# Kernel optimization log

Hardware: AMD Instinct MI355X
Metric: run time of the kernel (lower is better)

The kernel has to match this reference:

```python
import math
import jax, jax.numpy as jnp
import numpy as np

D_MODEL = 768
N_HEAD = 12
N_BR = 4
DH = D_MODEL // N_HEAD          # 64
H_TOT = N_BR * N_HEAD           # 48
SCALE = math.pi / math.sqrt(3.0)
ATTNSCALE = DH ** -0.5


def _chebyshev(T, max_deg, dtype):
    # T_all[t, d] = Cheb poly T_d(x_t), x in [-1, 1]
    if T > 1:
        x = 2.0 * jnp.arange(T, dtype=dtype) / (T - 1) - 1.0
    else:
        x = jnp.zeros(1, dtype=dtype)
    cols = [jnp.ones_like(x), x]
    for _ in range(2, max_deg + 1):
        cols.append(2.0 * x * cols[-1] - cols[-2])
    return jnp.stack(cols, axis=1)  # (T, max_deg+1)


def setup_inputs() -> dict:
    key = jax.random.key(0)
    ks = jax.random.split(key, 12)
    s = 0.02
    return {
        "X": jax.random.normal(ks[0], (2, 1024, D_MODEL), jnp.float32),
        "Wq": jax.random.normal(ks[1], (D_MODEL * N_BR, D_MODEL), jnp.float32) * s,
        "bq": jax.random.normal(ks[2], (D_MODEL * N_BR,), jnp.float32) * s,
        "Wk": jax.random.normal(ks[3], (D_MODEL, D_MODEL), jnp.float32) * s,
        "bk": jax.random.normal(ks[4], (D_MODEL,), jnp.float32) * s,
        "Wv": jax.random.normal(ks[5], (D_MODEL, D_MODEL), jnp.float32) * s,
        "bv": jax.random.normal(ks[6], (D_MODEL,), jnp.float32) * s,
        "A": jax.random.normal(ks[7], (DH, DH), jnp.float32) * s,
        "id_bias": jax.random.normal(ks[8], (H_TOT, DH), jnp.float32) * s,
        "sink_scalars": jax.random.normal(ks[9], (H_TOT, 1, 1), jnp.float32) * s,
        "v_nulls": jax.random.normal(ks[10], (N_BR, D_MODEL), jnp.float32) * s,
        "Wo": jax.random.normal(ks[11], (N_BR, D_MODEL, D_MODEL), jnp.float32) * s,
        "bo": jnp.zeros((N_BR, D_MODEL), jnp.float32),
    }


def _attention(X, Wq, bq, Wk, bk, Wv, bv, A, id_bias, sink_scalars, v_nulls, Wo, bo):
    B, T, C = X.shape
    dtype = X.dtype

    # projections (torch Linear: x @ W.T + b)
    q = (X @ Wq.T + bq).reshape(B, T, H_TOT, DH).transpose(0, 2, 1, 3)   # (B,H_tot,T,Dh)
    v = (X @ Wv.T + bv).reshape(B, T, N_HEAD, DH).transpose(0, 2, 1, 3)
    v = jnp.tile(v, (1, N_BR, 1, 1))                                     # (B,H_tot,T,Dh)
    k = (X @ Wk.T + bk).reshape(B, T, N_HEAD, DH).transpose(0, 2, 1, 3)
    k = jnp.tile(k, (1, N_BR, 1, 1))

    # BiasedWedge on q
    S = (A - A.T)[None] + jax.vmap(jnp.diag)(id_bias)                    # (H_tot,Dh,Dh)
    q = q + jnp.einsum('bhtd,hde->bhte', q, S)

    # Chebyshev phase-vector rotation (custom RoPE)
    H = DH // 2
    max_deg = max(3, 2 * H)
    T_all = _chebyshev(T, max_deg, dtype)                                # (T, max_deg+1)
    frac = jnp.arange(H, dtype=dtype) / (H - 1) if H > 1 else jnp.zeros(1, dtype)
    n_f = jnp.clip(1 + jnp.round(frac * (max_deg - 2)).astype(jnp.int32), 1, max_deg - 1)
    raw1 = T_all[:, n_f]                                                 # (T,H)
    raw2 = T_all[:, n_f + 1]
    nrm = jnp.sqrt(raw1 * raw1 + raw2 * raw2 + 1e-8)
    base1 = (raw1 / nrm)[None, None]                                     # (1,1,T,H)
    base2 = (raw2 / nrm)[None, None]

    def apply_rot(x_in):
        x1, x2 = x_in[..., :H], x_in[..., H:]
        return jnp.concatenate([x1 * base1 - x2 * base2,
                                x1 * base2 + x2 * base1], axis=-1)

    q = apply_rot(q)
    k = apply_rot(k)

    # softplus-gated causal attention with learned sink
    scores = jnp.einsum('bhtd,bhsd->bhts', q, k) * ATTNSCALE             # (B,H_tot,T,T)
    key_self = jnp.maximum((k * k).sum(-1), 1e-6)                        # (B,H_tot,T)
    denom = jnp.sqrt(key_self)[:, :, None, :]
    w = jax.nn.softplus(scores / denom)
    causal = jnp.tril(jnp.ones((T, T), bool))                            # keep lower-tri
    w = jnp.where(causal, w, 0.0)
    w = w * jax.nn.sigmoid(SCALE * w)

    sinks = sink_scalars.reshape(1, H_TOT, 1, 1)                         # broadcast sink col
    alpha = 1.0 / (w.sum(-1, keepdims=True) + sinks + 1e-6)              # (B,H_tot,T,1)
    probs_tokens = w * alpha
    probs_sink = jnp.broadcast_to(sinks, (B, H_TOT, T, 1)) * alpha

    out_tokens = jnp.einsum('bhts,bhsd->bhtd', probs_tokens, v)
    v_null = v_nulls.reshape(H_TOT, DH)[None, :, None, :]                # (1,H_tot,1,Dh)
    context = out_tokens + probs_sink * v_null                           # (B,H_tot,T,Dh)

    context = context.reshape(B, N_BR, N_HEAD, T, DH)
    context = context.transpose(0, 1, 3, 2, 4).reshape(B, N_BR, T, C)
    y = jnp.einsum('bntc,ncd->bntd', context, Wo) + bo[None, :, None, :]
    return y.mean(axis=1)                                                # (B,T,C)


def reference(X, Wq, bq, Wk, bk, Wv, bv, A, id_bias, sink_scalars, v_nulls, Wo, bo):
    return _attention(X, Wq, bq, Wk, bk, Wv, bv, A, id_bias, sink_scalars, v_nulls, Wo, bo)
```

## Files before the change

### kernel.cpp

```cpp
#include <hip/hip_runtime.h>
#include <math.h>

#define B_ 2
#define T_ 1024
#define C_ 768
#define NH 12
#define NBR 4
#define DH_ 64
#define HT 48
#define MROWS (B_*T_)

#define SCALE_W 1.8137993642342178f
#define ATTNSCALE_ 0.125f

#define OFF_B1    0
#define OFF_B2    (OFF_B1 + 32768)
#define OFF_QKVB  (OFF_B2 + 32768)
#define OFF_BSUM  (OFF_QKVB + 4608)
#define OFF_WQKV  (OFF_BSUM + 768)
#define OFF_XB    (OFF_WQKV + 1769472)
#define OFF_WOT   (OFF_XB + 786432)
#define OFF_QF    (OFF_WOT + 1179648)
#define OFF_KF    (OFF_QF + 6291456)
#define OFF_VF    (OFF_KF + 1572864)
#define OFF_QB    OFF_KF
#define OFF_KB    (OFF_VF + 1572864)
#define OFF_VB    (OFF_KB + 786432)
#define OFF_RKS   (OFF_VB + 786432)
#define OFF_CTXB  OFF_QF

typedef __attribute__((ext_vector_type(8))) short short8t;
typedef __attribute__((ext_vector_type(4))) float f32x4;

__device__ inline ushort f2bf(float f) {
    union { float f; unsigned u; } v; v.f = f;
    unsigned r = (v.u + 0x7FFFu + ((v.u >> 16) & 1u)) >> 16;
    return (ushort)r;
}

__global__ void cheb_kernel(float* __restrict__ ws) {
    int t = blockIdx.x * 256 + threadIdx.x;
    if (t >= T_) return;
    float* b1 = ws + OFF_B1 + t * 32;
    float* b2 = ws + OFF_B2 + t * 32;
    float x = 2.0f * (float)t / 1023.0f - 1.0f;
    float Tp = 1.0f, Tc = x;
    for (int j = 0; j < 32; j++) {
        float r1 = Tc;
        float r2 = 2.0f * x * Tc - Tp;
        float nr = sqrtf(r1 * r1 + r2 * r2 + 1e-8f);
        b1[j] = r1 / nr;
        b2[j] = r2 / nr;
        Tp = r2;
        Tc = 2.0f * x * r2 - r1;
    }
}

__global__ __launch_bounds__(256) void prep_wq(
    const float* __restrict__ Aw, const float* __restrict__ idb,
    const float* __restrict__ Wq, const float* __restrict__ bq,
    float* __restrict__ ws) {
    __shared__ float Ms[64][64];
    int h = blockIdx.x;
    int tid = threadIdx.x;
    for (int i = tid; i < 4096; i += 256) {
        int d = i >> 6, e = i & 63;
        float v = Aw[d * 64 + e] - Aw[e * 64 + d];
        if (d == e) v += 1.0f + idb[h * 64 + d];
        Ms[d][e] = v;
    }
    __syncthreads();
    int c = blockIdx.y * 256 + tid;
    float wq[64];
#pragma unroll
    for (int d = 0; d < 64; d++) wq[d] = Wq[(size_t)(h * 64 + d) * 768 + c];
    ushort* EWqb = (ushort*)(ws + OFF_WQKV);
    for (int e = 0; e < 64; e++) {
        float acc = 0.f;
#pragma unroll
        for (int d = 0; d < 64; d++) acc += Ms[d][e] * wq[d];
        EWqb[(size_t)(h * 64 + e) * 768 + c] = f2bf(acc);
    }
    if (blockIdx.y == 0 && tid < 64) {
        int e = tid;
        float acc = 0.f;
        for (int d = 0; d < 64; d++) acc += Ms[d][e] * bq[h * 64 + d];
        ws[OFF_QKVB + h * 64 + e] = acc;
    }
}

__global__ void conv_bf16(const float* __restrict__ src, ushort* __restrict__ dst) {
    int i = (blockIdx.x * 256 + threadIdx.x) * 4;
    float4 v = *(const float4*)(src + i);
    ushort4 o;
    o.x = f2bf(v.x); o.y = f2bf(v.y); o.z = f2bf(v.z); o.w = f2bf(v.w);
    *(ushort4*)(dst + i) = o;
}

__global__ __launch_bounds__(256) void woT_kernel(const float* __restrict__ Wo,
                                                  ushort* __restrict__ WoT) {
    __shared__ float tile[64][65];
    int nb = blockIdx.z;
    int k0 = blockIdx.x * 64, c0 = blockIdx.y * 64;
    int tx = threadIdx.x & 63, ty = threadIdx.x >> 6;
#pragma unroll
    for (int p = 0; p < 16; p++) {
        int ky = p * 4 + ty;
        tile[ky][tx] = Wo[((size_t)nb * 768 + k0 + ky) * 768 + c0 + tx];
    }
    __syncthreads();
#pragma unroll
    for (int p = 0; p < 16; p++) {
        int cy = p * 4 + ty;
        WoT[(size_t)(c0 + cy) * 3072 + nb * 768 + k0 + tx] = f2bf(tile[tx][cy]);
    }
}

__global__ void bias_prep(const float* __restrict__ bo, const float* __restrict__ bk,
                          const float* __restrict__ bv, float* __restrict__ ws) {
    int n = blockIdx.x * 256 + threadIdx.x;
    if (n < 768) {
        ws[OFF_BSUM + n] = 0.25f * (bo[n] + bo[768 + n] + bo[1536 + n] + bo[2304 + n]);
        ws[OFF_QKVB + 3072 + n] = bk[n];
        ws[OFF_QKVB + 3840 + n] = bv[n];
    }
}

__global__ __launch_bounds__(256) void gemm_qkv(
    const ushort* __restrict__ A, const ushort* __restrict__ Bw,
    const float* __restrict__ qkvbias,
    float* __restrict__ Q, float* __restrict__ Kf, float* __restrict__ Vf) {
    __shared__ __align__(16) ushort As[128][72];
    __shared__ __align__(16) ushort Bs[128][72];
    const int K = 768;
    int tid = threadIdx.x;
    int lane = tid & 63, wid = tid >> 6;
    int wr = wid >> 1, wc = wid & 1;
    int g = lane >> 4, c = lane & 15;
    int m0 = blockIdx.x * 128, n0 = blockIdx.y * 128;
    int srow = tid >> 3;
    int scol = (tid & 7) * 8;
    f32x4 acc[4][4] = {};
    for (int k0 = 0; k0 < K; k0 += 64) {
        __syncthreads();
#pragma unroll
        for (int p = 0; p < 4; p++) {
            int r = p * 32 + srow;
            *(int4*)&As[r][scol] = *(const int4*)(A + (size_t)(m0 + r) * K + k0 + scol);
            *(int4*)&Bs[r][scol] = *(const int4*)(Bw + (size_t)(n0 + r) * K + k0 + scol);
        }
        __syncthreads();
#pragma unroll
        for (int kk = 0; kk < 2; kk++) {
            short8t af[4], bf[4];
#pragma unroll
            for (int i = 0; i < 4; i++) {
                af[i] = *(const short8t*)&As[wr * 64 + i * 16 + c][kk * 32 + g * 8];
                bf[i] = *(const short8t*)&Bs[wc * 64 + i * 16 + c][kk * 32 + g * 8];
            }
#pragma unroll
            for (int i = 0; i < 4; i++)
#pragma unroll
                for (int j = 0; j < 4; j++)
                    acc[i][j] = __builtin_amdgcn_mfma_f32_16x16x32_bf16(
                        af[i], bf[j], acc[i][j], 0, 0, 0);
        }
    }
    int y = blockIdx.y;
    float* outp; int nstr, nbase;
    if (y < 24)      { outp = Q;  nstr = 3072; nbase = 0; }
    else if (y < 30) { outp = Kf; nstr = 768;  nbase = 3072; }
    else             { outp = Vf; nstr = 768;  nbase = 3840; }
#pragma unroll
    for (int j = 0; j < 4; j++) {
        int n = n0 + wc * 64 + j * 16 + c;
        float bv = qkvbias[n];
#pragma unroll
        for (int i = 0; i < 4; i++) {
#pragma unroll
            for (int r = 0; r < 4; r++) {
                int m = m0 + wr * 64 + i * 16 + g * 4 + r;
                outp[(size_t)m * nstr + (n - nbase)] = acc[i][j][r] + bv;
            }
        }
    }
}

__global__ __launch_bounds__(256) void gemm_fin(
    const ushort* __restrict__ A, const ushort* __restrict__ Bw,
    const float* __restrict__ bsum, float* __restrict__ Y) {
    __shared__ __align__(16) ushort As[64][72];
    __shared__ __align__(16) ushort Bs[64][72];
    const int K = 3072;
    int tid = threadIdx.x;
    int lane = tid & 63, wid = tid >> 6;
    int wr = wid >> 1, wc = wid & 1;
    int g = lane >> 4, c = lane & 15;
    int m0 = blockIdx.x * 64, n0 = blockIdx.y * 64;
    int srow = tid >> 2;
    int scol = (tid & 3) * 16;
    f32x4 acc[2][2] = {};
    for (int k0 = 0; k0 < K; k0 += 64) {
        __syncthreads();
        *(int4*)&As[srow][scol]     = *(const int4*)(A + (size_t)(m0 + srow) * K + k0 + scol);
        *(int4*)&As[srow][scol + 8] = *(const int4*)(A + (size_t)(m0 + srow) * K + k0 + scol + 8);
        *(int4*)&Bs[srow][scol]     = *(const int4*)(Bw + (size_t)(n0 + srow) * K + k0 + scol);
        *(int4*)&Bs[srow][scol + 8] = *(const int4*)(Bw + (size_t)(n0 + srow) * K + k0 + scol + 8);
        __syncthreads();
#pragma unroll
        for (int kk = 0; kk < 2; kk++) {
            short8t af[2], bf[2];
#pragma unroll
            for (int i = 0; i < 2; i++) {
                af[i] = *(const short8t*)&As[wr * 32 + i * 16 + c][kk * 32 + g * 8];
                bf[i] = *(const short8t*)&Bs[wc * 32 + i * 16 + c][kk * 32 + g * 8];
            }
#pragma unroll
            for (int i = 0; i < 2; i++)
#pragma unroll
                for (int j = 0; j < 2; j++)
                    acc[i][j] = __builtin_amdgcn_mfma_f32_16x16x32_bf16(
                        af[i], bf[j], acc[i][j], 0, 0, 0);
        }
    }
#pragma unroll
    for (int j = 0; j < 2; j++) {
        int n = n0 + wc * 32 + j * 16 + c;
        float bv = bsum[n];
#pragma unroll
        for (int i = 0; i < 2; i++) {
#pragma unroll
            for (int r = 0; r < 4; r++) {
                int m = m0 + wr * 32 + i * 16 + g * 4 + r;
                Y[(size_t)m * 768 + n] = 0.25f * acc[i][j][r] + bv;
            }
        }
    }
}

__global__ void rot2_kernel(const float* __restrict__ in, int heads,
                            ushort* __restrict__ outb, float* __restrict__ rkso,
                            const float* __restrict__ ws) {
    int idx = blockIdx.x * 256 + threadIdx.x;
    if (idx >= MROWS * heads) return;
    int r = idx / heads;
    int hd = idx - r * heads;
    int tloc = r & (T_ - 1);
    int b = r >> 10;
    const float* p = in + (size_t)r * (heads * 64) + hd * 64;
    const float* b1 = ws + OFF_B1 + tloc * 32;
    const float* b2 = ws + OFF_B2 + tloc * 32;
    __align__(16) ushort ob[64];
    float nrm = 0.f;
#pragma unroll
    for (int i = 0; i < 8; i++) {
        float4 lo = *(const float4*)(p + i * 4);
        float4 hi = *(const float4*)(p + 32 + i * 4);
        float4 c1 = *(const float4*)(b1 + i * 4);
        float4 c2 = *(const float4*)(b2 + i * 4);
        float o1[4], o2[4];
        o1[0] = lo.x * c1.x - hi.x * c2.x;  o2[0] = lo.x * c2.x + hi.x * c1.x;
        o1[1] = lo.y * c1.y - hi.y * c2.y;  o2[1] = lo.y * c2.y + hi.y * c1.y;
        o1[2] = lo.z * c1.z - hi.z * c2.z;  o2[2] = lo.z * c2.z + hi.z * c1.z;
        o1[3] = lo.w * c1.w - hi.w * c2.w;  o2[3] = lo.w * c2.w + hi.w * c1.w;
#pragma unroll
        for (int j = 0; j < 4; j++) {
            ob[i * 4 + j]      = f2bf(o1[j]);
            ob[32 + i * 4 + j] = f2bf(o2[j]);
            nrm += o1[j] * o1[j] + o2[j] * o2[j];
        }
    }
    ushort* op = outb + ((size_t)(b * heads + hd) * T_ + tloc) * 64;
#pragma unroll
    for (int i = 0; i < 8; i++) *(int4*)(op + i * 8) = *(const int4*)&ob[i * 8];
    if (rkso) rkso[((b * heads + hd) << 10) + tloc] = ATTNSCALE_ / sqrtf(fmaxf(nrm, 1e-6f));
}

__global__ void vconv_kernel(const float* __restrict__ V, ushort* __restrict__ Vb) {
    int idx = blockIdx.x * 256 + threadIdx.x;
    int base = idx * 4;
    int row = base / 768, col = base - row * 768;
    int b = row >> 10, t = row & (T_ - 1);
    int hk = col >> 6, d = col & 63;
    float4 v = *(const float4*)(V + (size_t)row * 768 + col);
    ushort4 o;
    o.x = f2bf(v.x); o.y = f2bf(v.y); o.z = f2bf(v.z); o.w = f2bf(v.w);
    *(ushort4*)(Vb + ((size_t)((b * NH + hk) * T_ + t)) * 64 + d) = o;
}

__global__ __launch_bounds__(512) void attn_mfma2(
    const ushort* __restrict__ Qb, const ushort* __restrict__ Kb,
    const ushort* __restrict__ Vb, const float* __restrict__ rks,
    const float* __restrict__ sinks, const float* __restrict__ vnull,
    ushort* __restrict__ ctxb) {
    __shared__ __align__(16) ushort Ks[64][72];
    __shared__ __align__(16) ushort Vt[64][72];
    __shared__ __align__(16) ushort Ps[8][16][72];
    __shared__ float rk_s[64];
    int tid  = threadIdx.x;
    int lane = tid & 63;
    int wid  = tid >> 6;
    int p = 7 - blockIdx.x;
    int bh = blockIdx.y;
    int b = bh / HT, h = bh - b * HT;
    int hk = h % NH;
    int qt0 = p * 128;
    int g = lane >> 4;
    int c = lane & 15;
    int rowbase = qt0 + wid * 16;

    const ushort* qrow = Qb + ((size_t)(b * HT + h) * T_ + rowbase + c) * 64;
    short8t qa0 = *(const short8t*)(qrow + g * 8);
    short8t qa1 = *(const short8t*)(qrow + 32 + g * 8);

    f32x4 oacc[4] = {};
    float sumw[4] = {0.f, 0.f, 0.f, 0.f};

    const size_t kvbase = (size_t)(b * NH + hk) * T_;
    int nt = 2 * p + 2;
    int sr = tid >> 3;
    int sc = (tid & 7) * 8;
    for (int st = 0; st < nt; st++) {
        int s0 = st * 64;
        __syncthreads();
        {
            *(int4*)&Ks[sr][sc] = *(const int4*)(Kb + (kvbase + s0 + sr) * 64 + sc);
            __align__(16) ushort vv[8];
            *(int4*)&vv[0] = *(const int4*)(Vb + (kvbase + s0 + sr) * 64 + sc);
#pragma unroll
            for (int j = 0; j < 8; j++) Vt[sc + j][sr] = vv[j];
            if (tid < 64) rk_s[tid] = rks[kvbase + (size_t)s0 + tid];
        }
        __syncthreads();

        if (s0 > rowbase + 15) continue;

        f32x4 sfr[4];
#pragma unroll
        for (int f = 0; f < 4; f++) {
            f32x4 cacc = {0.f, 0.f, 0.f, 0.f};
            short8t kb0 = *(const short8t*)&Ks[f * 16 + c][g * 8];
            cacc = __builtin_amdgcn_mfma_f32_16x16x32_bf16(qa0, kb0, cacc, 0, 0, 0);
            short8t kb1 = *(const short8t*)&Ks[f * 16 + c][32 + g * 8];
            cacc = __builtin_amdgcn_mfma_f32_16x16x32_bf16(qa1, kb1, cacc, 0, 0, 0);
            sfr[f] = cacc;
        }

        bool diag = (s0 + 63 > rowbase);
#pragma unroll
        for (int f = 0; f < 4; f++) {
            int scol = f * 16 + c;
            float rkv = rk_s[scol];
#pragma unroll
            for (int r = 0; r < 4; r++) {
                int trow = g * 4 + r;
                float x = sfr[f][r] * rkv;
                float w = __logf(1.f + __expf(x));
                w = w * __builtin_amdgcn_rcpf(1.f + __expf(-SCALE_W * w));
                if (diag && s0 + scol > rowbase + trow) w = 0.f;
                sumw[r] += w;
                Ps[wid][trow][scol] = f2bf(w);
            }
        }

#pragma unroll
        for (int hf = 0; hf < 2; hf++) {
            short8t pa = *(const short8t*)&Ps[wid][c][hf * 32 + g * 8];
#pragma unroll
            for (int f = 0; f < 4; f++) {
                short8t vb = *(const short8t*)&Vt[f * 16 + c][hf * 32 + g * 8];
                oacc[f] = __builtin_amdgcn_mfma_f32_16x16x32_bf16(pa, vb, oacc[f], 0, 0, 0);
            }
        }
    }

#pragma unroll
    for (int m = 1; m < 16; m <<= 1) {
#pragma unroll
        for (int r = 0; r < 4; r++) sumw[r] += __shfl_xor(sumw[r], m, 64);
    }
    float skv = sinks[h];
    float alpha[4], ps[4];
#pragma unroll
    for (int r = 0; r < 4; r++) {
        alpha[r] = 1.0f / (sumw[r] + skv + 1e-6f);
        ps[r] = skv * alpha[r];
    }
    int nb = h / NH;
#pragma unroll
    for (int f = 0; f < 4; f++) {
        float vn = vnull[h * 64 + f * 16 + c];
#pragma unroll
        for (int r = 0; r < 4; r++) {
            int t = rowbase + g * 4 + r;
            ctxb[(size_t)(b * T_ + t) * 3072 + nb * 768 + hk * 64 + f * 16 + c]
                = f2bf(oacc[f][r] * alpha[r] + ps[r] * vn);
        }
    }
}

extern "C" void kernel_launch(void* const* d_in, const int* in_sizes, int n_in,
                              void* d_out, int out_size, void* d_ws, size_t ws_size,
                              hipStream_t stream) {
    const float* X   = (const float*)d_in[0];
    const float* Wq  = (const float*)d_in[1];
    const float* bq  = (const float*)d_in[2];
    const float* Wk  = (const float*)d_in[3];
    const float* bk  = (const float*)d_in[4];
    const float* Wv  = (const float*)d_in[5];
    const float* bv  = (const float*)d_in[6];
    const float* Aw  = (const float*)d_in[7];
    const float* idb = (const float*)d_in[8];
    const float* sk  = (const float*)d_in[9];
    const float* vn  = (const float*)d_in[10];
    const float* Wo  = (const float*)d_in[11];
    const float* bo  = (const float*)d_in[12];
    float* ws = (float*)d_ws;
    float* Y  = (float*)d_out;

    ushort* WQKV = (ushort*)(ws + OFF_WQKV);
    hipLaunchKernelGGL(cheb_kernel, dim3(4), dim3(256), 0, stream, ws);
    hipLaunchKernelGGL(prep_wq, dim3(48, 3), dim3(256), 0, stream, Aw, idb, Wq, bq, ws);
    hipLaunchKernelGGL(conv_bf16, dim3(576), dim3(256), 0, stream,
                       Wk, WQKV + (size_t)3072 * 768);
    hipLaunchKernelGGL(conv_bf16, dim3(576), dim3(256), 0, stream,
                       Wv, WQKV + (size_t)3840 * 768);
    hipLaunchKernelGGL(conv_bf16, dim3(1536), dim3(256), 0, stream,
                       X, (ushort*)(ws + OFF_XB));
    hipLaunchKernelGGL(woT_kernel, dim3(12, 12, 4), dim3(256), 0, stream,
                       Wo, (ushort*)(ws + OFF_WOT));
    hipLaunchKernelGGL(bias_prep, dim3(3), dim3(256), 0, stream, bo, bk, bv, ws);
    hipLaunchKernelGGL(gemm_qkv, dim3(16, 36), dim3(256), 0, stream,
                       (const ushort*)(ws + OFF_XB), WQKV, ws + OFF_QKVB,
                       ws + OFF_QF, ws + OFF_KF, ws + OFF_VF);
    hipLaunchKernelGGL(rot2_kernel, dim3(96), dim3(256), 0, stream,
                       ws + OFF_KF, NH, (ushort*)(ws + OFF_KB), ws + OFF_RKS, ws);
    hipLaunchKernelGGL(vconv_kernel, dim3(1536), dim3(256), 0, stream,
                       ws + OFF_VF, (ushort*)(ws + OFF_VB));
    hipLaunchKernelGGL(rot2_kernel, dim3(384), dim3(256), 0, stream,
                       ws + OFF_QF, HT, (ushort*)(ws + OFF_QB), (float*)nullptr, ws);
    hipLaunchKernelGGL(attn_mfma2, dim3(8, 96), dim3(512), 0, stream,
                       (const ushort*)(ws + OFF_QB), (const ushort*)(ws + OFF_KB),
                       (const ushort*)(ws + OFF_VB), ws + OFF_RKS, sk, vn,
                       (ushort*)(ws + OFF_CTXB));
    hipLaunchKernelGGL(gemm_fin, dim3(32, 12), dim3(256), 0, stream,
                       (const ushort*)(ws + OFF_CTXB), (const ushort*)(ws + OFF_WOT),
                       ws + OFF_BSUM, Y);
}
```

Baseline: 341.4 us.

## Use direct global-to-LDS loads with swizzle and split-K atomics for output GEMM

Both GEMMs now share a k-loop that loads tiles straight from global memory into LDS with global_load_lds and an XOR-swizzled layout, replacing the register-staged copies and the padded arrays. The final projection GEMM moves from 64x64 tiles to 128x128 tiles split three ways along K, accumulating into Y with atomic adds after a new kernel pre-fills Y with the bias. This is meant to cut LDS bank conflicts and load instruction overhead and to raise arithmetic intensity while keeping enough blocks busy. The cost is an extra launch, float atomics whose summation order is not deterministic, and a loop that still has no double buffering.

```diff
diff --git a/kernel.cpp b/kernel.cpp
--- a/kernel.cpp
+++ b/kernel.cpp
@@ -38,6 +38,12 @@
     return (ushort)r;
 }
 
+typedef __attribute__((address_space(3))) void lds_vt;
+typedef const __attribute__((address_space(1))) void gbl_vt;
+static __device__ __forceinline__ void gload16(const void* g, void* l) {
+    __builtin_amdgcn_global_load_lds((gbl_vt*)g, (lds_vt*)l, 16, 0, 0);
+}
+
 __global__ void cheb_kernel(float* __restrict__ ws) {
     int t = blockIdx.x * 256 + threadIdx.x;
     if (t >= T_) return;
@@ -126,46 +132,74 @@
     }
 }
 
+__global__ void y_init(const float* __restrict__ bsum, float* __restrict__ Y) {
+    int idx = (blockIdx.x * 256 + threadIdx.x) * 4;
+    int n = idx - (idx / 768) * 768;
+    float4 o = { bsum[n], bsum[n + 1], bsum[n + 2], bsum[n + 3] };
+    *(float4*)(Y + idx) = o;
+}
+
+static __device__ __forceinline__ void gemm_kloop128(
+    const ushort* __restrict__ A, const ushort* __restrict__ B, int K,
+    int m0, int n0, int k_begin, int k_end,
+    ushort* AsU, ushort* BsU, f32x4 acc[4][4], int tid) {
+    char* As = (char*)AsU;
+    char* Bs = (char*)BsU;
+    int lane = tid & 63, w = tid >> 6;
+    int g = lane >> 4, c = lane & 15;
+    int wr = w >> 1, wc = w & 1;
+    int srow[4], scol[4];
+#pragma unroll
+    for (int r = 0; r < 4; r++) {
+        int p = r * 4096 + w * 1024 + lane * 16;
+        int row = p >> 7;
+        int bp = (p & 127) ^ ((row & 7) << 4);
+        srow[r] = row;
+        scol[r] = bp >> 1;
+    }
+    for (int k0 = k_begin; k0 < k_end; k0 += 64) {
+        __syncthreads();
+#pragma unroll
+        for (int r = 0; r < 4; r++) {
+            gload16(A + (size_t)(m0 + srow[r]) * K + k0 + scol[r],
+                    As + r * 4096 + w * 1024);
+            gload16(B + (size_t)(n0 + srow[r]) * K + k0 + scol[r],
+                    Bs + r * 4096 + w * 1024);
+        }
+        __syncthreads();
+#pragma unroll
+        for (int kk = 0; kk < 2; kk++) {
+            short8t af[4], bf[4];
+#pragma unroll
+            for (int i = 0; i < 4; i++) {
+                int ra = wr * 64 + i * 16 + c;
+                af[i] = *(const short8t*)(As + ra * 128 + ((kk * 64 + g * 16) ^ ((ra & 7) << 4)));
+                int rb = wc * 64 + i * 16 + c;
+                bf[i] = *(const short8t*)(Bs + rb * 128 + ((kk * 64 + g * 16) ^ ((rb & 7) << 4)));
+            }
+#pragma unroll
+            for (int i = 0; i < 4; i++)
+#pragma unroll
+                for (int j = 0; j < 4; j++)
+                    acc[i][j] = __builtin_amdgcn_mfma_f32_16x16x32_bf16(
+                        af[i], bf[j], acc[i][j], 0, 0, 0);
+        }
+    }
+}
+
 __global__ __launch_bounds__(256) void gemm_qkv(
     const ushort* __restrict__ A, const ushort* __restrict__ Bw,
     const float* __restrict__ qkvbias,
     float* __restrict__ Q, float* __restrict__ Kf, float* __restrict__ Vf) {
-    __shared__ __align__(16) ushort As[128][72];
-    __shared__ __align__(16) ushort Bs[128][72];
-    const int K = 768;
+    __shared__ __align__(16) ushort AsU[8192];
+    __shared__ __align__(16) ushort BsU[8192];
     int tid = threadIdx.x;
     int lane = tid & 63, wid = tid >> 6;
     int wr = wid >> 1, wc = wid & 1;
     int g = lane >> 4, c = lane & 15;
     int m0 = blockIdx.x * 128, n0 = blockIdx.y * 128;
-    int srow = tid >> 3;
-    int scol = (tid & 7) * 8;
     f32x4 acc[4][4] = {};
-    for (int k0 = 0; k0 < K; k0 += 64) {
-        __syncthreads();
-#pragma unroll
-        for (int p = 0; p < 4; p++) {
-            int r = p * 32 + srow;
-            *(int4*)&As[r][scol] = *(const int4*)(A + (size_t)(m0 + r) * K + k0 + scol);
-            *(int4*)&Bs[r][scol] = *(const int4*)(Bw + (size_t)(n0 + r) * K + k0 + scol);
-        }
-        __syncthreads();
-#pragma unroll
-        for (int kk = 0; kk < 2; kk++) {
-            short8t af[4], bf[4];
-#pragma unroll
-            for (int i = 0; i < 4; i++) {
-                af[i] = *(const short8t*)&As[wr * 64 + i * 16 + c][kk * 32 + g * 8];
-                bf[i] = *(const short8t*)&Bs[wc * 64 + i * 16 + c][kk * 32 + g * 8];
-            }
-#pragma unroll
-            for (int i = 0; i < 4; i++)
-#pragma unroll
-                for (int j = 0; j < 4; j++)
-                    acc[i][j] = __builtin_amdgcn_mfma_f32_16x16x32_bf16(
-                        af[i], bf[j], acc[i][j], 0, 0, 0);
-        }
-    }
+    gemm_kloop128(A, Bw, 768, m0, n0, 0, 768, AsU, BsU, acc, tid);
     int y = blockIdx.y;
     float* outp; int nstr, nbase;
     if (y < 24)      { outp = Q;  nstr = 3072; nbase = 0; }
@@ -188,51 +222,26 @@
 
 __global__ __launch_bounds__(256) void gemm_fin(
     const ushort* __restrict__ A, const ushort* __restrict__ Bw,
-    const float* __restrict__ bsum, float* __restrict__ Y) {
-    __shared__ __align__(16) ushort As[64][72];
-    __shared__ __align__(16) ushort Bs[64][72];
-    const int K = 3072;
+    float* __restrict__ Y) {
+    __shared__ __align__(16) ushort AsU[8192];
+    __shared__ __align__(16) ushort BsU[8192];
     int tid = threadIdx.x;
     int lane = tid & 63, wid = tid >> 6;
     int wr = wid >> 1, wc = wid & 1;
     int g = lane >> 4, c = lane & 15;
-    int m0 = blockIdx.x * 64, n0 = blockIdx.y * 64;
-    int srow = tid >> 2;
-    int scol = (tid & 3) * 16;
-    f32x4 acc[2][2] = {};
-    for (int k0 = 0; k0 < K; k0 += 64) {
-        __syncthreads();
-        *(int4*)&As[srow][scol]     = *(const int4*)(A + (size_t)(m0 + srow) * K + k0 + scol);
-        *(int4*)&As[srow][scol + 8] = *(const int4*)(A + (size_t)(m0 + srow) * K + k0 + scol + 8);
-        *(int4*)&Bs[srow][scol]     = *(const int4*)(Bw + (size_t)(n0 + srow) * K + k0 + scol);
-        *(int4*)&Bs[srow][scol + 8] = *(const int4*)(Bw + (size_t)(n0 + srow) * K + k0 + scol + 8);
-        __syncthreads();
-#pragma unroll
-        for (int kk = 0; kk < 2; kk++) {
-            short8t af[2], bf[2];
-#pragma unroll
-            for (int i = 0; i < 2; i++) {
-                af[i] = *(const short8t*)&As[wr * 32 + i * 16 + c][kk * 32 + g * 8];
-                bf[i] = *(const short8t*)&Bs[wc * 32 + i * 16 + c][kk * 32 + g * 8];
-            }
-#pragma unroll
-            for (int i = 0; i < 2; i++)
-#pragma unroll
-                for (int j = 0; j < 2; j++)
-                    acc[i][j] = __builtin_amdgcn_mfma_f32_16x16x32_bf16(
-                        af[i], bf[j], acc[i][j], 0, 0, 0);
-        }
-    }
-#pragma unroll
-    for (int j = 0; j < 2; j++) {
-        int n = n0 + wc * 32 + j * 16 + c;
-        float bv = bsum[n];
-#pragma unroll
-        for (int i = 0; i < 2; i++) {
+    int m0 = blockIdx.x * 128, n0 = blockIdx.y * 128;
+    int kz = blockIdx.z * 1024;
+    f32x4 acc[4][4] = {};
+    gemm_kloop128(A, Bw, 3072, m0, n0, kz, kz + 1024, AsU, BsU, acc, tid);
+#pragma unroll
+    for (int j = 0; j < 4; j++) {
+        int n = n0 + wc * 64 + j * 16 + c;
+#pragma unroll
+        for (int i = 0; i < 4; i++) {
 #pragma unroll
             for (int r = 0; r < 4; r++) {
-                int m = m0 + wr * 32 + i * 16 + g * 4 + r;
-                Y[(size_t)m * 768 + n] = 0.25f * acc[i][j][r] + bv;
+                int m = m0 + wr * 64 + i * 16 + g * 4 + r;
+                atomicAdd(&Y[(size_t)m * 768 + n], 0.25f * acc[i][j][r]);
             }
         }
     }
@@ -443,7 +452,7 @@
                        (const ushort*)(ws + OFF_QB), (const ushort*)(ws + OFF_KB),
                        (const ushort*)(ws + OFF_VB), ws + OFF_RKS, sk, vn,
                        (ushort*)(ws + OFF_CTXB));
-    hipLaunchKernelGGL(gemm_fin, dim3(32, 12), dim3(256), 0, stream,
-                       (const ushort*)(ws + OFF_CTXB), (const ushort*)(ws + OFF_WOT),
-                       ws + OFF_BSUM, Y);
-}
+    hipLaunchKernelGGL(y_init, dim3(1536), dim3(256), 0, stream, ws + OFF_BSUM, Y);
+    hipLaunchKernelGGL(gemm_fin, dim3(16, 6, 3), dim3(256), 0, stream,
+                       (const ushort*)(ws + OFF_CTXB), (const ushort*)(ws + OFF_WOT), Y);
+}
```

Result: faster. 328.4 us (-3.8%).
